# Kernel tuning notes

Measured on AMD Instinct MI355X. Metric: run time of the kernel, lower is better.

The kernel has to match this reference:

```python
import jax, jax.numpy as jnp
import numpy as np

# config constants
S = 26            # output_size (fm_width == fm_height)
A = 5             # anchor_num
C = 80            # class_num
B = 64            # batch_size
T = 16            # GT boxes per image
DS = 32.0         # downsample_rate
IOU_THR = 0.5
SCALE_NOOBJ = 1.0
SCALE_OBJ = 5.0
ANCHOR_BOX = np.array([[1.32, 1.73], [3.19, 4.0], [5.05, 8.09], [9.47, 4.84], [11.2, 10.0]], dtype=np.float32)


def setup_inputs() -> dict:
    key = jax.random.key(0)
    ks = jax.random.split(key, 8)
    conf = jax.random.normal(ks[0], (B, S, S, A, 1), dtype=jnp.float32)
    pred_xy = jax.random.uniform(ks[1], (B, S, S, A, 2), dtype=jnp.float32) * S
    pred_wh = jax.random.uniform(ks[2], (B, S, S, A, 2), dtype=jnp.float32) * S + 0.5
    cls_score = jax.random.normal(ks[3], (B, S, S, A, C), dtype=jnp.float32)
    # GT boxes in PIXEL coords (module divides by downsample_rate): (x, y, w, h)
    xy = jax.random.uniform(ks[4], (B, T, 2), dtype=jnp.float32) * (S * DS)
    wh = jax.random.uniform(ks[5], (B, T, 2), dtype=jnp.float32) * (S * DS * 0.5) + DS
    true_object = jnp.concatenate([xy, wh], axis=-1)
    cls_idx = jax.random.randint(ks[6], (B, T), 0, C)
    true_label = jax.nn.one_hot(cls_idx, C, dtype=jnp.float32)
    # per-cell integer coords, row-major over the S*S grid
    p = jnp.arange(S * S)
    fm_cord = jnp.stack([p // S, p % S], axis=-1).astype(jnp.float32)  # [S*S, 2]
    anchors = jnp.asarray(ANCHOR_BOX)
    epoch = 1
    return {"epoch": epoch, "conf": conf, "pred_xy": pred_xy, "pred_wh": pred_wh,
            "cls_score": cls_score, "true_object": true_object, "true_label": true_label,
            "fm_cord": fm_cord, "anchors": anchors}


def _center_align_iou_wh(wh1, wh2):
    # IoU of two boxes whose centers are aligned: only (w, h) matter.
    inter = jnp.minimum(wh1[..., 0], wh2[..., 0]) * jnp.minimum(wh1[..., 1], wh2[..., 1])
    union = wh1[..., 0] * wh1[..., 1] + wh2[..., 0] * wh2[..., 1] - inter
    return inter / union


def _bce_with_logits(x, t):
    return jnp.maximum(x, 0.0) - x * t + jnp.log1p(jnp.exp(-jnp.abs(x)))


def _assign_targets(pred_wh, true_object, true_label, anchors):
    """Vectorized replacement of the per-box Python loops."""
    g = true_object / DS                                   # [B,T,4] in fm units
    gw, gh = g[..., 2], g[..., 3]
    i = jnp.clip(jnp.floor(g[..., 0]).astype(jnp.int32), 0, S - 1)  # int(x)
    j = jnp.clip(jnp.floor(g[..., 1]).astype(jnp.int32), 0, S - 1)  # int(y)
    b_idx = jnp.broadcast_to(jnp.arange(B)[:, None], (B, T))

    # anchor-vs-gt center-aligned IoU: [B,T,A]
    inter = jnp.minimum(gw[..., None], anchors[:, 0]) * jnp.minimum(gh[..., None], anchors[:, 1])
    union = (gw * gh)[..., None] + anchors[:, 0] * anchors[:, 1] - inter
    iou_a = inter / union
    best = jnp.argmax(iou_a, axis=-1)                      # [B,T]

    # predicted box at the BEST anchor cell (the original uses best_iou_index in
    # both the if- and else- branches), center-aligned IoU against the gt box
    pbest_wh = pred_wh[b_idx, i, j, best]                  # [B,T,2]
    iou_pg = _center_align_iou_wh(pbest_wh, g[..., 2:4])   # [B,T]

    aa = jnp.broadcast_to(jnp.arange(A), (B, T, A))
    is_best = aa == best[..., None]
    over = iou_a > IOU_THR
    scale_best = 2.0 - (gw / S) * (gh / S)                 # [B,T]

    mask_val = jnp.where(is_best, 1.0, jnp.where(over, -1.0, 0.0))
    scale_val = jnp.where(is_best, scale_best[..., None], jnp.where(over, -1.0, 0.0))

    bi = jnp.broadcast_to(b_idx[..., None], (B, T, A))
    ii = jnp.broadcast_to(i[..., None], (B, T, A))
    jj = jnp.broadcast_to(j[..., None], (B, T, A))

    obj_mask = jnp.zeros((B, S, S, A), jnp.float32).at[bi, ii, jj, aa].set(mask_val)
    scale_weight = jnp.zeros((B, S, S, A), jnp.float32).at[bi, ii, jj, aa].set(scale_val)

    # pred_gt_iou is written for the best anchor and for non-best anchors BELOW
    # the threshold (else-branch); over-threshold non-best anchors are skipped.
    write_iou = is_best | (~over)
    a_safe = jnp.where(write_iou, aa, A)  # out-of-bounds -> dropped
    pred_gt_iou = jnp.zeros((B, S, S, A), jnp.float32).at[bi, ii, jj, a_safe].set(
        jnp.broadcast_to(iou_pg[..., None], (B, T, A)), mode="drop")

    true_bbox = jnp.zeros((B, S, S, A, 4), jnp.float32).at[b_idx, i, j, best].set(g)
    true_score = jnp.zeros((B, S, S, A, C), jnp.float32).at[..., -1].set(1.0)
    true_score = true_score.at[b_idx, i, j, best].set(true_label)
    return obj_mask, scale_weight, pred_gt_iou, true_bbox, true_score


def _yolo_loss(epoch, conf, pred_xy, pred_wh, cls_score, true_object, true_label, fm_cord, anchors):
    obj_mask, scale_weight, pred_gt_iou, true_bbox, true_score = _assign_targets(
        pred_wh, true_object, true_label, anchors)

    N = S * S * A
    conf_f = conf.reshape(B, N, 1)
    pxy = pred_xy.reshape(B, N, 2)
    pwh = pred_wh.reshape(B, N, 2)
    tb = true_bbox.reshape(B, N, 4)
    m = obj_mask.reshape(B, N, 1)
    piou = pred_gt_iou.reshape(B, N, 1)
    sw = scale_weight.reshape(B, N, 1)
    ts = true_score.reshape(B, N, C).transpose(0, 2, 1)    # [B,C,N]
    cs = cls_score.reshape(B, N, C).transpose(0, 2, 1)     # [B,C,N]
    # mimics fm_cord.view(WH,2).repeat(1,A,1): whole grid tiled A times -> [N,2]
    fm = jnp.tile(fm_cord, (A, 1))

    noobj_loss = (SCALE_NOOBJ * (m == 0) * 0.5 * conf_f ** 2).sum() / B
    obj_loss = (SCALE_OBJ * (m == 1) * 0.5 * (conf_f - piou) ** 2).sum() / B
    gt_mask = (sw > 0).astype(conf.dtype)
    true_loss_xy = (SCALE_OBJ * 0.5 * gt_mask * sw *
                    _bce_with_logits(pxy - fm[None], tb[..., :2] - fm[None])).sum() / B
    true_loss_wh = (SCALE_OBJ * 0.5 * gt_mask * sw * (pwh - tb[..., 2:]) ** 2).sum() / B
    cls_gt_mask = gt_mask.transpose(0, 2, 1)               # [B,1,N]
    score_loss = (SCALE_OBJ * 0.5 * cls_gt_mask * (cs - ts) ** 2).sum() / B
    # NOTE: original code computes the averaged total then OVERWRITES it:
    total_loss = score_loss
    return (total_loss, noobj_loss / 4.0, obj_loss / 4.0, score_loss / 4.0,
            true_loss_xy / 4.0, true_loss_wh / 4.0)


def reference(epoch, conf, pred_xy, pred_wh, cls_score, true_object, true_label, fm_cord, anchors):
    return _yolo_loss(epoch, conf, pred_xy, pred_wh, cls_score, true_object, true_label, fm_cord, anchors)
```

## Files before the change

kernel.cpp:

```cpp
#include <hip/hip_runtime.h>
#include <math.h>

#define S 26
#define A 5
#define C 80
#define B 64
#define T 16
#define DSR 32.0f
#define N_CELLS (S * S)
#define N_PRED (S * S * A)
#define CONF_N (B * N_PRED)
#define CONF_N4 (CONF_N / 4)
#define NBT (B * T)
#define NBLK 256

__global__ __launch_bounds__(256) void fused_main(
        const float* __restrict__ conf,
        const float* __restrict__ pred_xy,
        const float* __restrict__ pred_wh,
        const float* __restrict__ cls_score,
        const float* __restrict__ true_object,
        const float* __restrict__ true_label,
        const float* __restrict__ anchors,
        float* __restrict__ partials) {
    const int tid = threadIdx.x;
    const int bid = blockIdx.x;
    const int gidx = bid * 256 + tid;

    float v0 = 0.f, v1 = 0.f, v2 = 0.f, v3 = 0.f, v4 = 0.f, v5 = 0.f;

    if (gidx < CONF_N4) {
        float4 c = ((const float4*)conf)[gidx];
        v0 = c.x * c.x + c.y * c.y + c.z * c.z + c.w * c.w;
    }

    if (gidx < NBT) {
        const int b = gidx / T;
        const int t = gidx % T;

        const float* to = true_object + (size_t)(b * T + t) * 4;
        float gx = to[0] / DSR, gy = to[1] / DSR;
        float gw = to[2] / DSR, gh = to[3] / DSR;
        int i = (int)floorf(gx); i = min(max(i, 0), S - 1);
        int j = (int)floorf(gy); j = min(max(j, 0), S - 1);

        bool winner = true;
        for (int t2 = t + 1; t2 < T; ++t2) {
            const float* to2 = true_object + (size_t)(b * T + t2) * 4;
            int i2 = (int)floorf(to2[0] / DSR); i2 = min(max(i2, 0), S - 1);
            int j2 = (int)floorf(to2[1] / DSR); j2 = min(max(j2, 0), S - 1);
            if (i2 == i && j2 == j) { winner = false; break; }
        }

        if (winner) {
            float iou_a[A];
            int best = 0;
            float bestv = -1.f;
            for (int a = 0; a < A; ++a) {
                float aw = anchors[a * 2 + 0], ah = anchors[a * 2 + 1];
                float inter = fminf(gw, aw) * fminf(gh, ah);
                float uni = gw * gh + aw * ah - inter;
                float val = inter / uni;
                iou_a[a] = val;
                if (val > bestv) { bestv = val; best = a; }
            }

            size_t base = (size_t)b * N_PRED + (size_t)(i * S + j) * A;

            for (int a = 0; a < A; ++a) {
                if (a == best || iou_a[a] > 0.5f) {
                    float c = conf[base + a];
                    v1 += 0.5f * c * c;
                }
            }

            float pw = pred_wh[(base + best) * 2 + 0];
            float ph = pred_wh[(base + best) * 2 + 1];
            float inter = fminf(pw, gw) * fminf(ph, gh);
            float uni = pw * ph + gw * gh - inter;
            float iou_pg = inter / uni;
            float cbest = conf[base + best];
            float d = cbest - iou_pg;
            v2 = 0.5f * d * d;

            float sw = 2.0f - (gw / (float)S) * (gh / (float)S);
            if (sw > 0.f) {
                int n = (i * S + j) * A + best;
                int p = n % N_CELLS;
                float fm0 = (float)(p / S);
                float fm1 = (float)(p % S);
                float px = pred_xy[(base + best) * 2 + 0];
                float py = pred_xy[(base + best) * 2 + 1];
                float x0 = px - fm0, t0 = gx - fm0;
                float x1 = py - fm1, t1 = gy - fm1;
                float bce0 = fmaxf(x0, 0.f) - x0 * t0 + log1pf(expf(-fabsf(x0)));
                float bce1 = fmaxf(x1, 0.f) - x1 * t1 + log1pf(expf(-fabsf(x1)));
                v3 = sw * (bce0 + bce1);
                float dw = pw - gw, dh = ph - gh;
                v4 = sw * (dw * dw + dh * dh);

                const float* cs = cls_score + (base + best) * C;
                const float* tl = true_label + (size_t)(b * T + t) * C;
                float sacc = 0.f;
                for (int c = 0; c < C; ++c) {
                    float dd = cs[c] - tl[c];
                    sacc += dd * dd;
                }
                v5 = sacc;
            }
        }
    }

    float vs[6] = {v0, v1, v2, v3, v4, v5};
    #pragma unroll
    for (int k = 0; k < 6; ++k) {
        float v = vs[k];
        #pragma unroll
        for (int off = 32; off >= 1; off >>= 1)
            v += __shfl_xor(v, off, 64);
        vs[k] = v;
    }
    __shared__ float sm[4 * 6];
    const int wave = tid >> 6;
    const int lane = tid & 63;
    if (lane == 0) {
        #pragma unroll
        for (int k = 0; k < 6; ++k) sm[wave * 6 + k] = vs[k];
    }
    __syncthreads();
    if (tid < 6) {
        partials[tid * NBLK + bid] =
            sm[0 * 6 + tid] + sm[1 * 6 + tid] + sm[2 * 6 + tid] + sm[3 * 6 + tid];
    }
}

__global__ __launch_bounds__(64) void finalize_kernel(
        const float* __restrict__ partials, float* __restrict__ out) {
    const int tid = threadIdx.x;
    float sums[6];
    #pragma unroll
    for (int k = 0; k < 6; ++k) {
        const float* p = partials + k * NBLK;
        float v = p[tid] + p[tid + 64] + p[tid + 128] + p[tid + 192];
        #pragma unroll
        for (int off = 32; off >= 1; off >>= 1)
            v += __shfl_xor(v, off, 64);
        sums[k] = v;
    }

    if (tid == 0) {
        const float invB = 1.0f / (float)B;
        float noobj = (0.5f * sums[0] - sums[1]) * invB;
        float obj   = 5.0f * sums[2] * invB;
        float xy    = 5.0f * 0.5f * sums[3] * invB;
        float wh    = 5.0f * 0.5f * sums[4] * invB;
        float score = 5.0f * 0.5f * sums[5] * invB;
        out[0] = score;
        out[1] = noobj * 0.25f;
        out[2] = obj * 0.25f;
        out[3] = score * 0.25f;
        out[4] = xy * 0.25f;
        out[5] = wh * 0.25f;
    }
}

extern "C" void kernel_launch(void* const* d_in, const int* in_sizes, int n_in,
                              void* d_out, int out_size, void* d_ws, size_t ws_size,
                              hipStream_t stream) {
    const float* conf        = (const float*)d_in[1];
    const float* pred_xy     = (const float*)d_in[2];
    const float* pred_wh     = (const float*)d_in[3];
    const float* cls_score   = (const float*)d_in[4];
    const float* true_object = (const float*)d_in[5];
    const float* true_label  = (const float*)d_in[6];
    const float* anchors     = (const float*)d_in[8];

    float* ws  = (float*)d_ws;
    float* out = (float*)d_out;

    hipLaunchKernelGGL(fused_main, dim3(NBLK), dim3(256), 0, stream,
                       conf, pred_xy, pred_wh, cls_score, true_object,
                       true_label, anchors, ws);
    hipLaunchKernelGGL(finalize_kernel, dim3(1), dim3(64), 0, stream, ws, out);
}
```

Baseline: 15.54 us.

## Fuse main and finalize kernels via cooperative grid sync with vectorized loads

Merges the reduction and finalize kernels into one cooperative launch of 64 blocks of 1024 threads, using a grid-wide sync so block 0 does the final sum. This removes the second kernel launch, with a fallback to two launches if the cooperative launch fails. GT-box work now runs on threads separate from the conf-square threads. The winner check uses wave shuffles instead of re-reading neighbours. GT, pred and class-score loads are vectorized as float2 and float4. The risks are the cost of the grid barrier and the cooperative-launch overhead, plus the fewer, larger blocks.

```diff
diff --git a/kernel.cpp b/kernel.cpp
--- a/kernel.cpp
+++ b/kernel.cpp
@@ -1,5 +1,8 @@
 #include <hip/hip_runtime.h>
+#include <hip/hip_cooperative_groups.h>
 #include <math.h>
+
+namespace cg = cooperative_groups;
 
 #define S 26
 #define A 5
@@ -12,9 +15,12 @@
 #define CONF_N (B * N_PRED)
 #define CONF_N4 (CONF_N / 4)
 #define NBT (B * T)
-#define NBLK 256
-
-__global__ __launch_bounds__(256) void fused_main(
+#define NBLK 64
+#define BS 1024
+#define NWAVE (BS / 64)
+
+__device__ __forceinline__ void compute_terms(
+        int gidx,
         const float* __restrict__ conf,
         const float* __restrict__ pred_xy,
         const float* __restrict__ pred_wh,
@@ -22,40 +28,37 @@
         const float* __restrict__ true_object,
         const float* __restrict__ true_label,
         const float* __restrict__ anchors,
-        float* __restrict__ partials) {
-    const int tid = threadIdx.x;
-    const int bid = blockIdx.x;
-    const int gidx = bid * 256 + tid;
-
-    float v0 = 0.f, v1 = 0.f, v2 = 0.f, v3 = 0.f, v4 = 0.f, v5 = 0.f;
+        float vs[6]) {
+    vs[0] = vs[1] = vs[2] = vs[3] = vs[4] = vs[5] = 0.f;
 
     if (gidx < CONF_N4) {
         float4 c = ((const float4*)conf)[gidx];
-        v0 = c.x * c.x + c.y * c.y + c.z * c.z + c.w * c.w;
-    }
-
-    if (gidx < NBT) {
-        const int b = gidx / T;
-        const int t = gidx % T;
-
-        const float* to = true_object + (size_t)(b * T + t) * 4;
-        float gx = to[0] / DSR, gy = to[1] / DSR;
-        float gw = to[2] / DSR, gh = to[3] / DSR;
-        int i = (int)floorf(gx); i = min(max(i, 0), S - 1);
-        int j = (int)floorf(gy); j = min(max(j, 0), S - 1);
+        vs[0] = c.x * c.x + c.y * c.y + c.z * c.z + c.w * c.w;
+    } else if (gidx < CONF_N4 + NBT) {
+        const int bt = gidx - CONF_N4;
+        const int b = bt >> 4;
+        const int t = bt & 15;
+        const int lane = gidx & 63;
+
+        float4 to = ((const float4*)true_object)[bt];
+        float gx = to.x / DSR, gy = to.y / DSR;
+        float gw = to.z / DSR, gh = to.w / DSR;
+        int i = min(max((int)floorf(gx), 0), S - 1);
+        int j = min(max((int)floorf(gy), 0), S - 1);
+        int ij = i * S + j;
 
         bool winner = true;
-        for (int t2 = t + 1; t2 < T; ++t2) {
-            const float* to2 = true_object + (size_t)(b * T + t2) * 4;
-            int i2 = (int)floorf(to2[0] / DSR); i2 = min(max(i2, 0), S - 1);
-            int j2 = (int)floorf(to2[1] / DSR); j2 = min(max(j2, 0), S - 1);
-            if (i2 == i && j2 == j) { winner = false; break; }
+        #pragma unroll
+        for (int t2 = 0; t2 < T; ++t2) {
+            int ij2 = __shfl(ij, (lane & 48) + t2, 64);
+            if (t2 > t && ij2 == ij) winner = false;
         }
 
         if (winner) {
             float iou_a[A];
             int best = 0;
             float bestv = -1.f;
+            #pragma unroll
             for (int a = 0; a < A; ++a) {
                 float aw = anchors[a * 2 + 0], ah = anchors[a * 2 + 1];
                 float inter = fminf(gw, aw) * fminf(gh, ah);
@@ -65,53 +68,59 @@
                 if (val > bestv) { bestv = val; best = a; }
             }
 
-            size_t base = (size_t)b * N_PRED + (size_t)(i * S + j) * A;
-
+            size_t base = (size_t)b * N_PRED + (size_t)ij * A;
+
+            #pragma unroll
             for (int a = 0; a < A; ++a) {
                 if (a == best || iou_a[a] > 0.5f) {
                     float c = conf[base + a];
-                    v1 += 0.5f * c * c;
+                    vs[1] += 0.5f * c * c;
                 }
             }
 
-            float pw = pred_wh[(base + best) * 2 + 0];
-            float ph = pred_wh[(base + best) * 2 + 1];
+            float2 pwh = ((const float2*)pred_wh)[base + best];
+            float pw = pwh.x, ph = pwh.y;
             float inter = fminf(pw, gw) * fminf(ph, gh);
             float uni = pw * ph + gw * gh - inter;
             float iou_pg = inter / uni;
             float cbest = conf[base + best];
             float d = cbest - iou_pg;
-            v2 = 0.5f * d * d;
+            vs[2] = 0.5f * d * d;
 
             float sw = 2.0f - (gw / (float)S) * (gh / (float)S);
             if (sw > 0.f) {
-                int n = (i * S + j) * A + best;
+                int n = ij * A + best;
                 int p = n % N_CELLS;
                 float fm0 = (float)(p / S);
                 float fm1 = (float)(p % S);
-                float px = pred_xy[(base + best) * 2 + 0];
-                float py = pred_xy[(base + best) * 2 + 1];
-                float x0 = px - fm0, t0 = gx - fm0;
-                float x1 = py - fm1, t1 = gy - fm1;
-                float bce0 = fmaxf(x0, 0.f) - x0 * t0 + log1pf(expf(-fabsf(x0)));
-                float bce1 = fmaxf(x1, 0.f) - x1 * t1 + log1pf(expf(-fabsf(x1)));
-                v3 = sw * (bce0 + bce1);
+                float2 pxy = ((const float2*)pred_xy)[base + best];
+                float x0 = pxy.x - fm0, tt0 = gx - fm0;
+                float x1 = pxy.y - fm1, tt1 = gy - fm1;
+                float bce0 = fmaxf(x0, 0.f) - x0 * tt0 + log1pf(expf(-fabsf(x0)));
+                float bce1 = fmaxf(x1, 0.f) - x1 * tt1 + log1pf(expf(-fabsf(x1)));
+                vs[3] = sw * (bce0 + bce1);
                 float dw = pw - gw, dh = ph - gh;
-                v4 = sw * (dw * dw + dh * dh);
-
-                const float* cs = cls_score + (base + best) * C;
-                const float* tl = true_label + (size_t)(b * T + t) * C;
+                vs[4] = sw * (dw * dw + dh * dh);
+
+                const float4* cs4 = (const float4*)(cls_score + (base + best) * C);
+                const float4* tl4 = (const float4*)(true_label + (size_t)bt * C);
                 float sacc = 0.f;
-                for (int c = 0; c < C; ++c) {
-                    float dd = cs[c] - tl[c];
-                    sacc += dd * dd;
+                #pragma unroll
+                for (int c4 = 0; c4 < C / 4; ++c4) {
+                    float4 cc = cs4[c4];
+                    float4 tl = tl4[c4];
+                    float d0 = cc.x - tl.x, d1 = cc.y - tl.y;
+                    float d2 = cc.z - tl.z, d3 = cc.w - tl.w;
+                    sacc += d0 * d0 + d1 * d1 + d2 * d2 + d3 * d3;
                 }
-                v5 = sacc;
+                vs[5] = sacc;
             }
         }
     }
-
-    float vs[6] = {v0, v1, v2, v3, v4, v5};
+}
+
+__device__ __forceinline__ void block_reduce_write(
+        float vs[6], float* __restrict__ partials, int bid, int tid) {
     #pragma unroll
     for (int k = 0; k < 6; ++k) {
         float v = vs[k];
@@ -120,7 +129,7 @@
             v += __shfl_xor(v, off, 64);
         vs[k] = v;
     }
-    __shared__ float sm[4 * 6];
+    __shared__ float sm[NWAVE * 6];
     const int wave = tid >> 6;
     const int lane = tid & 63;
     if (lane == 0) {
@@ -129,32 +138,31 @@
     }
     __syncthreads();
     if (tid < 6) {
-        partials[tid * NBLK + bid] =
-            sm[0 * 6 + tid] + sm[1 * 6 + tid] + sm[2 * 6 + tid] + sm[3 * 6 + tid];
-    }
-}
-
-__global__ __launch_bounds__(64) void finalize_kernel(
-        const float* __restrict__ partials, float* __restrict__ out) {
-    const int tid = threadIdx.x;
+        float s = 0.f;
+        #pragma unroll
+        for (int w = 0; w < NWAVE; ++w) s += sm[w * 6 + tid];
+        partials[tid * NBLK + bid] = s;
+    }
+}
+
+__device__ __forceinline__ void finalize(
+        const float* __restrict__ partials, float* __restrict__ out, int tid) {
     float sums[6];
     #pragma unroll
     for (int k = 0; k < 6; ++k) {
-        const float* p = partials + k * NBLK;
-        float v = p[tid] + p[tid + 64] + p[tid + 128] + p[tid + 192];
+        float v = partials[k * NBLK + tid];
         #pragma unroll
         for (int off = 32; off >= 1; off >>= 1)
             v += __shfl_xor(v, off, 64);
         sums[k] = v;
     }
-
     if (tid == 0) {
         const float invB = 1.0f / (float)B;
         float noobj = (0.5f * sums[0] - sums[1]) * invB;
         float obj   = 5.0f * sums[2] * invB;
-        float xy    = 5.0f * 0.5f * sums[3] * invB;
-        float wh    = 5.0f * 0.5f * sums[4] * invB;
-        float score = 5.0f * 0.5f * sums[5] * invB;
+        float xy    = 2.5f * sums[3] * invB;
+        float wh    = 2.5f * sums[4] * invB;
+        float score = 2.5f * sums[5] * invB;
         out[0] = score;
         out[1] = noobj * 0.25f;
         out[2] = obj * 0.25f;
@@ -162,6 +170,40 @@
         out[4] = xy * 0.25f;
         out[5] = wh * 0.25f;
     }
+}
+
+__global__ __launch_bounds__(BS) void coop_kernel(
+        const float* __restrict__ conf, const float* __restrict__ pred_xy,
+        const float* __restrict__ pred_wh, const float* __restrict__ cls_score,
+        const float* __restrict__ true_object, const float* __restrict__ true_label,
+        const float* __restrict__ anchors, float* __restrict__ partials,
+        float* __restrict__ out) {
+    const int tid = threadIdx.x;
+    const int bid = blockIdx.x;
+    float vs[6];
+    compute_terms(bid * BS + tid, conf, pred_xy, pred_wh, cls_score,
+                  true_object, true_label, anchors, vs);
+    block_reduce_write(vs, partials, bid, tid);
+    cg::this_grid().sync();
+    if (bid == 0 && tid < 64) finalize(partials, out, tid);
+}
+
+__global__ __launch_bounds__(BS) void fb_main(
+        const float* __restrict__ conf, const float* __restrict__ pred_xy,
+        const float* __restrict__ pred_wh, const float* __restrict__ cls_score,
+        const float* __restrict__ true_object, const float* __restrict__ true_label,
+        const float* __restrict__ anchors, float* __restrict__ partials) {
+    const int tid = threadIdx.x;
+    const int bid = blockIdx.x;
+    float vs[6];
+    compute_terms(bid * BS + tid, conf, pred_xy, pred_wh, cls_score,
+                  true_object, true_label, anchors, vs);
+    block_reduce_write(vs, partials, bid, tid);
+}
+
+__global__ __launch_bounds__(64) void fb_finalize(
+        const float* __restrict__ partials, float* __restrict__ out) {
+    finalize(partials, out, threadIdx.x);
 }
 
 extern "C" void kernel_launch(void* const* d_in, const int* in_sizes, int n_in,
@@ -178,8 +220,17 @@
     float* ws  = (float*)d_ws;
     float* out = (float*)d_out;
 
-    hipLaunchKernelGGL(fused_main, dim3(NBLK), dim3(256), 0, stream,
-                       conf, pred_xy, pred_wh, cls_score, true_object,
-                       true_label, anchors, ws);
-    hipLaunchKernelGGL(finalize_kernel, dim3(1), dim3(64), 0, stream, ws, out);
-}
+    void* kargs[] = {(void*)&conf, (void*)&pred_xy, (void*)&pred_wh,
+                     (void*)&cls_score, (void*)&true_object, (void*)&true_label,
+                     (void*)&anchors, (void*)&ws, (void*)&out};
+    hipError_t e = hipLaunchCooperativeKernel((const void*)coop_kernel,
+                                              dim3(NBLK), dim3(BS), kargs, 0,
+                                              stream);
+    if (e != hipSuccess) {
+        (void)hipGetLastError();
+        hipLaunchKernelGGL(fb_main, dim3(NBLK), dim3(BS), 0, stream,
+                           conf, pred_xy, pred_wh, cls_score, true_object,
+                           true_label, anchors, ws);
+        hipLaunchKernelGGL(fb_finalize, dim3(1), dim3(64), 0, stream, ws, out);
+    }
+}
```

Measured after the change: 47.33 us. +204.6%, slower.
